# Kernel tuning notes

Measured on AMD Instinct MI355X. Metric: run time of the kernel, lower is better.

Reference implementation:

```python
import jax, jax.numpy as jnp
import numpy as np

NUM_USERS = 100000
NUM_ITEMS = 50000
EMB_DIM = 128
N_EDGES = 1600000
BATCH = 16384
L_USER = (0, 1, 2)


def setup_inputs() -> dict:
    key = jax.random.key(0)
    k1, k2, k3, k4, k5, k6 = jax.random.split(key, 6)
    users = jax.random.randint(k1, (BATCH,), 0, NUM_USERS)
    items = jax.random.randint(k2, (BATCH,), 0, NUM_ITEMS)
    edge_src = jax.random.randint(k3, (N_EDGES,), 0, NUM_USERS)
    edge_dst = jax.random.randint(k4, (N_EDGES,), 0, NUM_USERS)
    # nn.Parameter init: normal(mean=0, std=0.01)
    user_emb = jax.random.normal(k5, (NUM_USERS, EMB_DIM), dtype=jnp.float32) * 0.01
    item_emb = jax.random.normal(k6, (NUM_ITEMS, EMB_DIM), dtype=jnp.float32) * 0.01
    return {"users": users, "items": items, "edge_src": edge_src,
            "edge_dst": edge_dst, "user_emb": user_emb, "item_emb": item_emb}


def social_conv(edge_src, edge_dst, h):
    # DGL copy_u -> mean aggregation over social (user-user) edges
    msgs = h[edge_src]  # [E, D] gather
    agg = jax.ops.segment_sum(msgs, edge_dst, num_segments=NUM_USERS)  # [N, D]
    deg = jax.ops.segment_sum(jnp.ones_like(edge_dst, dtype=h.dtype), edge_dst,
                              num_segments=NUM_USERS)  # [N]
    return agg / jnp.maximum(deg, 1.0)[:, None]


def reference(users, items, edge_src, edge_dst, user_emb, item_emb):
    g1 = social_conv(edge_src, edge_dst, user_emb)
    g2 = social_conv(edge_src, edge_dst, g1)
    final_user = jnp.zeros_like(user_emb)
    if 0 in L_USER:
        final_user = final_user + user_emb
    if 1 in L_USER:
        final_user = final_user + g1
    if 2 in L_USER:
        final_user = final_user + g2
    latest_user = final_user[users]   # [B, D]
    latest_item = item_emb[items]     # [B, D]
    predict = jax.nn.sigmoid(jnp.sum(latest_user * latest_item, axis=1))  # [B]
    return predict, latest_user, latest_item
```

## Files before the change

### kernel.cpp

```cpp
#include <hip/hip_runtime.h>
#include <math.h>

#define NUM_USERS 100000
#define NUM_ITEMS 50000
#define EMB_D 128
#define N_EDGES 1600000
#define BATCH 16384

#define NBINS 782
#define CHUNK 8192
#define NCHUNKS 196
#define CELL 32
#define CAP 64
#define BINSZ (NCHUNKS * CELL)
#define SENT 0xFFFFFFFFu

#define CVT_BLOCKS 782
#define BMAP_BLOCKS 16
#define N_F4 3200000

#define FP8_SCALE 512.0f
#define FP8_INV   (1.0f / 512.0f)

typedef unsigned int u32;
typedef float f32x2 __attribute__((ext_vector_type(2)));

__device__ __forceinline__ long long g18row(int u) {
    return (long long)(u >> 7) * BINSZ + (long long)(u & 127) * 32;
}

__global__ __launch_bounds__(1024) void prep_kernel(const float* __restrict__ in,
                            u32* __restrict__ outp, const int* __restrict__ users,
                            u32* __restrict__ bitmap,
                            const int* __restrict__ edge_src, const int* __restrict__ edge_dst,
                            u32* __restrict__ coarse) {
    int blk = blockIdx.x;
    int tid = threadIdx.x;
    if (blk >= NCHUNKS) {
        int cb = blk - NCHUNKS;
        if (cb < CVT_BLOCKS) {
            long long bbase = (long long)cb * 4096;
            float4 a[4];
            #pragma unroll
            for (int g = 0; g < 4; g++) {
                long long i = bbase + g * 1024 + tid;
                if (i < N_F4) a[g] = ((const float4*)in)[i];
            }
            #pragma unroll
            for (int g = 0; g < 4; g++) {
                long long i = bbase + g * 1024 + tid;
                if (i < N_F4) {
                    int r = __builtin_amdgcn_cvt_pk_fp8_f32(a[g].x * FP8_SCALE,
                                                            a[g].y * FP8_SCALE, 0, false);
                    r = __builtin_amdgcn_cvt_pk_fp8_f32(a[g].z * FP8_SCALE,
                                                        a[g].w * FP8_SCALE, r, true);
                    outp[i] = (u32)r;
                }
            }
        } else {
            int i = (cb - CVT_BLOCKS) * 1024 + tid;
            if (i < BATCH) {
                int u = users[i];
                atomicOr(&bitmap[u >> 5], 1u << (u & 31));
            }
        }
        return;
    }
    extern __shared__ u32 sm[];
    u32* cells = sm;
    int* cnt2  = (int*)(sm + NBINS * CELL);
    for (int i = tid; i < NBINS * CELL; i += 1024) cells[i] = SENT;
    for (int i = tid; i < NBINS; i += 1024) cnt2[i] = 0;
    __syncthreads();
    long long c0 = (long long)blk * CHUNK;
    int n = (int)min((long long)CHUNK, (long long)N_EDGES - c0);
    int n4 = n >> 2;
    const int4* d4p = (const int4*)(edge_dst + c0);
    const int4* s4p = (const int4*)(edge_src + c0);
    for (int i = tid; i < n4; i += 1024) {
        int4 d = d4p[i];
        int4 s = s4p[i];
        int dd[4] = {d.x, d.y, d.z, d.w};
        int ss[4] = {s.x, s.y, s.z, s.w};
        #pragma unroll
        for (int k = 0; k < 4; k++) {
            int b = dd[k] >> 7;
            int idx = atomicAdd(&cnt2[b], 1);
            if (idx < CELL)
                cells[b * CELL + idx] = ((u32)ss[k] << 7) | (u32)(dd[k] & 127);
        }
    }
    __syncthreads();
    const int I4 = NBINS * (CELL / 4);
    for (int i4 = tid; i4 < I4; i4 += 1024) {
        int bin = i4 >> 3;
        int off = i4 & 7;
        *(uint4*)(coarse + (long long)bin * BINSZ + blk * CELL + off * 4) =
            ((const uint4*)cells)[i4];
    }
}

__global__ void binagg_kernel(u32* __restrict__ coarse, const u32* __restrict__ tab32,
                              const u32* __restrict__ bitmap,
                              int* __restrict__ srt, int* __restrict__ counts) {
    __shared__ int cur[128];
    __shared__ int stage[128 * 65];
    int b = blockIdx.x;
    int tid = threadIdx.x;
    if (tid < 128) cur[tid] = 0;
    __syncthreads();
    const uint4* col = (const uint4*)(coarse + (long long)b * BINSZ);
    for (int i4 = tid; i4 < BINSZ / 4; i4 += 512) {
        uint4 q4 = col[i4];
        u32 pv[4] = {q4.x, q4.y, q4.z, q4.w};
        #pragma unroll
        for (int k = 0; k < 4; k++) {
            u32 p = pv[k];
            if (p != SENT) {
                int dl = (int)(p & 127u);
                int pos = atomicAdd(&cur[dl], 1);
                if (pos < CAP) stage[dl * 65 + pos] = (int)(p >> 7);
            }
        }
    }
    __syncthreads();
    int binBase = b << 7;
    int wv = tid >> 6;
    int lane = tid & 63;
    int dlane = lane & 31;
    int hi = lane >> 5;
    for (int dl = wv; dl < 128; dl += 8) {
        int user = binBase + dl;
        if (user >= NUM_USERS) continue;
        int cnt = cur[dl];
        int cl = min(cnt, CAP);
        int sbase = dl * 65;
        float4 acc = make_float4(0.f, 0.f, 0.f, 0.f);
        int j = 0;
        for (; j + 16 <= cl; j += 16) {
            int rr[8];
            #pragma unroll
            for (int k = 0; k < 8; k++) {
                int s0 = stage[sbase + j + 2 * k];
                int s1 = stage[sbase + j + 2 * k + 1];
                rr[k] = hi ? s1 : s0;
            }
            u32 pp[8];
            #pragma unroll
            for (int k = 0; k < 8; k++) pp[k] = tab32[(long long)rr[k] * 32 + dlane];
            #pragma unroll
            for (int k = 0; k < 8; k++) {
                f32x2 d0 = __builtin_amdgcn_cvt_pk_f32_fp8((int)pp[k], false);
                f32x2 d1 = __builtin_amdgcn_cvt_pk_f32_fp8((int)pp[k], true);
                acc.x += d0.x; acc.y += d0.y; acc.z += d1.x; acc.w += d1.y;
            }
        }
        if (j < cl) {
            int rr[8]; float ww[8];
            #pragma unroll
            for (int k = 0; k < 8; k++) {
                int i0 = min(j + 2 * k, cl - 1);
                int i1 = min(j + 2 * k + 1, cl - 1);
                int s0 = stage[sbase + i0];
                int s1 = stage[sbase + i1];
                rr[k] = hi ? s1 : s0;
                ww[k] = ((j + 2 * k + hi) < cl) ? 1.0f : 0.0f;
            }
            u32 pp[8];
            #pragma unroll
            for (int k = 0; k < 8; k++) pp[k] = tab32[(long long)rr[k] * 32 + dlane];
            #pragma unroll
            for (int k = 0; k < 8; k++) {
                f32x2 d0 = __builtin_amdgcn_cvt_pk_f32_fp8((int)pp[k], false);
                f32x2 d1 = __builtin_amdgcn_cvt_pk_f32_fp8((int)pp[k], true);
                acc.x += d0.x * ww[k]; acc.y += d0.y * ww[k];
                acc.z += d1.x * ww[k]; acc.w += d1.y * ww[k];
            }
        }
        acc.x += __shfl_xor(acc.x, 32, 64);
        acc.y += __shfl_xor(acc.y, 32, 64);
        acc.z += __shfl_xor(acc.z, 32, 64);
        acc.w += __shfl_xor(acc.w, 32, 64);
        float inv = 1.0f / fmaxf((float)cnt, 1.0f);
        int enc = __builtin_amdgcn_cvt_pk_fp8_f32(acc.x * inv, acc.y * inv, 0, false);
        enc = __builtin_amdgcn_cvt_pk_fp8_f32(acc.z * inv, acc.w * inv, enc, true);
        if (lane < 32) coarse[g18row(user) + dlane] = (u32)enc;
        if ((bitmap[user >> 5] >> (user & 31)) & 1u)
            srt[(long long)user * CAP + lane] = stage[sbase + lane];
        if (lane == 0) counts[user] = cnt;
    }
}

__global__ void final_kernel(const int* __restrict__ users, const int* __restrict__ items,
                             const float* __restrict__ user_emb, const float* __restrict__ item_emb,
                             const u32* __restrict__ g18, const int* __restrict__ counts,
                             const int* __restrict__ srt,
                             float* __restrict__ out_predict, float* __restrict__ out_lu,
                             float* __restrict__ out_li) {
    int b = (blockIdx.x * blockDim.x + threadIdx.x) >> 6;
    int lane = threadIdx.x & 63;
    if (b >= BATCH) return;
    b = __builtin_amdgcn_readfirstlane(b);
    int u = users[b];
    int it = items[b];
    int cnt = counts[u];
    int cl = min(cnt, CAP);
    long long start = (long long)u * CAP;
    int dlane = lane & 31;
    int hi = lane >> 5;
    float4 acc = make_float4(0.f, 0.f, 0.f, 0.f);
    int j = 0;
    for (; j + 16 <= cl; j += 16) {
        int rr[8];
        #pragma unroll
        for (int k = 0; k < 8; k++) {
            int s0 = srt[start + j + 2 * k];
            int s1 = srt[start + j + 2 * k + 1];
            rr[k] = hi ? s1 : s0;
        }
        u32 pp[8];
        #pragma unroll
        for (int k = 0; k < 8; k++) pp[k] = g18[g18row(rr[k]) + dlane];
        #pragma unroll
        for (int k = 0; k < 8; k++) {
            f32x2 d0 = __builtin_amdgcn_cvt_pk_f32_fp8((int)pp[k], false);
            f32x2 d1 = __builtin_amdgcn_cvt_pk_f32_fp8((int)pp[k], true);
            acc.x += d0.x; acc.y += d0.y; acc.z += d1.x; acc.w += d1.y;
        }
    }
    if (j < cl) {
        int rr[8]; float ww[8];
        #pragma unroll
        for (int k = 0; k < 8; k++) {
            int i0 = min(j + 2 * k, cl - 1);
            int i1 = min(j + 2 * k + 1, cl - 1);
            int s0 = srt[start + i0];
            int s1 = srt[start + i1];
            rr[k] = hi ? s1 : s0;
            ww[k] = ((j + 2 * k + hi) < cl) ? 1.0f : 0.0f;
        }
        u32 pp[8];
        #pragma unroll
        for (int k = 0; k < 8; k++) pp[k] = g18[g18row(rr[k]) + dlane];
        #pragma unroll
        for (int k = 0; k < 8; k++) {
            f32x2 d0 = __builtin_amdgcn_cvt_pk_f32_fp8((int)pp[k], false);
            f32x2 d1 = __builtin_amdgcn_cvt_pk_f32_fp8((int)pp[k], true);
            acc.x += d0.x * ww[k]; acc.y += d0.y * ww[k];
            acc.z += d1.x * ww[k]; acc.w += d1.y * ww[k];
        }
    }
    acc.x += __shfl_xor(acc.x, 32, 64);
    acc.y += __shfl_xor(acc.y, 32, 64);
    acc.z += __shfl_xor(acc.z, 32, 64);
    acc.w += __shfl_xor(acc.w, 32, 64);
    float inv = (1.0f / fmaxf((float)cnt, 1.0f)) * FP8_INV;
    float4 ue = *(const float4*)(user_emb + (long long)u * EMB_D + dlane * 4);
    u32 a1p = g18[g18row(u) + dlane];
    f32x2 a0 = __builtin_amdgcn_cvt_pk_f32_fp8((int)a1p, false);
    f32x2 a1 = __builtin_amdgcn_cvt_pk_f32_fp8((int)a1p, true);
    float4 ie = *(const float4*)(item_emb + (long long)it * EMB_D + dlane * 4);
    float4 lu;
    lu.x = ue.x + a0.x * FP8_INV + acc.x * inv;
    lu.y = ue.y + a0.y * FP8_INV + acc.y * inv;
    lu.z = ue.z + a1.x * FP8_INV + acc.z * inv;
    lu.w = ue.w + a1.y * FP8_INV + acc.w * inv;
    if (lane < 32) {
        *(float4*)(out_lu + (long long)b * EMB_D + dlane * 4) = lu;
        *(float4*)(out_li + (long long)b * EMB_D + dlane * 4) = ie;
    }
    float dot = lu.x * ie.x + lu.y * ie.y + lu.z * ie.z + lu.w * ie.w;
    #pragma unroll
    for (int off = 16; off > 0; off >>= 1) dot += __shfl_down(dot, off, 64);
    if (lane == 0) out_predict[b] = 1.0f / (1.0f + expf(-dot));
}

extern "C" void kernel_launch(void* const* d_in, const int* in_sizes, int n_in,
                              void* d_out, int out_size, void* d_ws, size_t ws_size,
                              hipStream_t stream) {
    const int* users     = (const int*)d_in[0];
    const int* items     = (const int*)d_in[1];
    const int* edge_src  = (const int*)d_in[2];
    const int* edge_dst  = (const int*)d_in[3];
    const float* user_emb = (const float*)d_in[4];
    const float* item_emb = (const float*)d_in[5];

    const long long COARSE_U32 = (long long)NBINS * BINSZ;
    const int SMEM_PART = (NBINS * CELL + NBINS) * 4;

    int* ws_i = (int*)d_ws;
    int* counts = ws_i;
    int* srt    = counts + 100352;
    u32* ue8    = (u32*)(srt + (long long)NUM_USERS * CAP);
    u32* coarse = ue8 + 3200000;
    u32* bitmap = coarse + COARSE_U32;

    float* out_predict = (float*)d_out;
    float* out_lu = out_predict + BATCH;
    float* out_li = out_lu + (long long)BATCH * EMB_D;

    static int lds_set = 0;
    if (!lds_set) {
        hipFuncSetAttribute((const void*)prep_kernel,
                            hipFuncAttributeMaxDynamicSharedMemorySize, SMEM_PART);
        lds_set = 1;
    }

    hipMemsetAsync(bitmap, 0, 3200 * sizeof(u32), stream);

    prep_kernel<<<NCHUNKS + CVT_BLOCKS + BMAP_BLOCKS, 1024, SMEM_PART, stream>>>(
        user_emb, ue8, users, bitmap, edge_src, edge_dst, coarse);

    binagg_kernel<<<NBINS, 512, 0, stream>>>(coarse, ue8, bitmap, srt, counts);

    final_kernel<<<(BATCH + 3) / 4, 256, 0, stream>>>(
        users, items, user_emb, item_emb, coarse, counts, srt,
        out_predict, out_lu, out_li);
}
```

Before: 204.3 us.

## Split bin aggregation into half-bins and compact g1 and neighbor-list storage

The bin aggregation kernel now runs two blocks per destination bin, each handling 64 users, which doubles the grid and halves the shared staging. The cost is that each block reads the whole coarse column and discards half of it. g1 is written to a separate dense fp8 table instead of being folded back into the coarse buffer, so addressing becomes a simple row index. Per-user neighbor lists are stored only for batch users, compacted through a slot map set with atomicMin. This adds a memset and an extra indirection in the final kernel.

```diff
diff --git a/kernel.cpp b/kernel.cpp
--- a/kernel.cpp
+++ b/kernel.cpp
@@ -8,6 +8,7 @@
 #define BATCH 16384
 
 #define NBINS 782
+#define NHALF 1564
 #define CHUNK 8192
 #define NCHUNKS 196
 #define CELL 32
@@ -25,13 +26,9 @@
 typedef unsigned int u32;
 typedef float f32x2 __attribute__((ext_vector_type(2)));
 
-__device__ __forceinline__ long long g18row(int u) {
-    return (long long)(u >> 7) * BINSZ + (long long)(u & 127) * 32;
-}
-
 __global__ __launch_bounds__(1024) void prep_kernel(const float* __restrict__ in,
                             u32* __restrict__ outp, const int* __restrict__ users,
-                            u32* __restrict__ bitmap,
+                            u32* __restrict__ bitmap, int* __restrict__ slot,
                             const int* __restrict__ edge_src, const int* __restrict__ edge_dst,
                             u32* __restrict__ coarse) {
     int blk = blockIdx.x;
@@ -62,6 +59,7 @@
             if (i < BATCH) {
                 int u = users[i];
                 atomicOr(&bitmap[u >> 5], 1u << (u & 31));
+                atomicMin(&slot[u], i);
             }
         }
         return;
@@ -100,16 +98,21 @@
     }
 }
 
-__global__ void binagg_kernel(u32* __restrict__ coarse, const u32* __restrict__ tab32,
-                              const u32* __restrict__ bitmap,
-                              int* __restrict__ srt, int* __restrict__ counts) {
-    __shared__ int cur[128];
-    __shared__ int stage[128 * 65];
+__global__ void binagg_kernel(const u32* __restrict__ coarse, const u32* __restrict__ tab32,
+                              const u32* __restrict__ bitmap, const int* __restrict__ slot,
+                              u32* __restrict__ g18, int* __restrict__ srt,
+                              int* __restrict__ counts) {
+    __shared__ int cur[64];
+    __shared__ int stage[64 * 65];
     int b = blockIdx.x;
+    int bin = b >> 1;
+    int h = b & 1;
+    int binBase = (bin << 7) + (h << 6);
+    if (binBase >= NUM_USERS) return;
     int tid = threadIdx.x;
-    if (tid < 128) cur[tid] = 0;
+    if (tid < 64) cur[tid] = 0;
     __syncthreads();
-    const uint4* col = (const uint4*)(coarse + (long long)b * BINSZ);
+    const uint4* col = (const uint4*)(coarse + (long long)bin * BINSZ);
     for (int i4 = tid; i4 < BINSZ / 4; i4 += 512) {
         uint4 q4 = col[i4];
         u32 pv[4] = {q4.x, q4.y, q4.z, q4.w};
@@ -118,18 +121,20 @@
             u32 p = pv[k];
             if (p != SENT) {
                 int dl = (int)(p & 127u);
-                int pos = atomicAdd(&cur[dl], 1);
-                if (pos < CAP) stage[dl * 65 + pos] = (int)(p >> 7);
+                if ((dl >> 6) == h) {
+                    int d = dl & 63;
+                    int pos = atomicAdd(&cur[d], 1);
+                    if (pos < CAP) stage[d * 65 + pos] = (int)(p >> 7);
+                }
             }
         }
     }
     __syncthreads();
-    int binBase = b << 7;
     int wv = tid >> 6;
     int lane = tid & 63;
     int dlane = lane & 31;
     int hi = lane >> 5;
-    for (int dl = wv; dl < 128; dl += 8) {
+    for (int dl = wv; dl < 64; dl += 8) {
         int user = binBase + dl;
         if (user >= NUM_USERS) continue;
         int cnt = cur[dl];
@@ -184,9 +189,11 @@
         float inv = 1.0f / fmaxf((float)cnt, 1.0f);
         int enc = __builtin_amdgcn_cvt_pk_fp8_f32(acc.x * inv, acc.y * inv, 0, false);
         enc = __builtin_amdgcn_cvt_pk_fp8_f32(acc.z * inv, acc.w * inv, enc, true);
-        if (lane < 32) coarse[g18row(user) + dlane] = (u32)enc;
-        if ((bitmap[user >> 5] >> (user & 31)) & 1u)
-            srt[(long long)user * CAP + lane] = stage[sbase + lane];
+        if (lane < 32) g18[(long long)user * 32 + dlane] = (u32)enc;
+        if ((bitmap[user >> 5] >> (user & 31)) & 1u) {
+            int s = slot[user];
+            srt[(long long)s * CAP + lane] = stage[sbase + lane];
+        }
         if (lane == 0) counts[user] = cnt;
     }
 }
@@ -194,7 +201,7 @@
 __global__ void final_kernel(const int* __restrict__ users, const int* __restrict__ items,
                              const float* __restrict__ user_emb, const float* __restrict__ item_emb,
                              const u32* __restrict__ g18, const int* __restrict__ counts,
-                             const int* __restrict__ srt,
+                             const int* __restrict__ slot, const int* __restrict__ srt,
                              float* __restrict__ out_predict, float* __restrict__ out_lu,
                              float* __restrict__ out_li) {
     int b = (blockIdx.x * blockDim.x + threadIdx.x) >> 6;
@@ -205,7 +212,7 @@
     int it = items[b];
     int cnt = counts[u];
     int cl = min(cnt, CAP);
-    long long start = (long long)u * CAP;
+    long long start = (long long)slot[u] * CAP;
     int dlane = lane & 31;
     int hi = lane >> 5;
     float4 acc = make_float4(0.f, 0.f, 0.f, 0.f);
@@ -220,7 +227,7 @@
         }
         u32 pp[8];
         #pragma unroll
-        for (int k = 0; k < 8; k++) pp[k] = g18[g18row(rr[k]) + dlane];
+        for (int k = 0; k < 8; k++) pp[k] = g18[(long long)rr[k] * 32 + dlane];
         #pragma unroll
         for (int k = 0; k < 8; k++) {
             f32x2 d0 = __builtin_amdgcn_cvt_pk_f32_fp8((int)pp[k], false);
@@ -241,7 +248,7 @@
         }
         u32 pp[8];
         #pragma unroll
-        for (int k = 0; k < 8; k++) pp[k] = g18[g18row(rr[k]) + dlane];
+        for (int k = 0; k < 8; k++) pp[k] = g18[(long long)rr[k] * 32 + dlane];
         #pragma unroll
         for (int k = 0; k < 8; k++) {
             f32x2 d0 = __builtin_amdgcn_cvt_pk_f32_fp8((int)pp[k], false);
@@ -256,7 +263,7 @@
     acc.w += __shfl_xor(acc.w, 32, 64);
     float inv = (1.0f / fmaxf((float)cnt, 1.0f)) * FP8_INV;
     float4 ue = *(const float4*)(user_emb + (long long)u * EMB_D + dlane * 4);
-    u32 a1p = g18[g18row(u) + dlane];
+    u32 a1p = g18[(long long)u * 32 + dlane];
     f32x2 a0 = __builtin_amdgcn_cvt_pk_f32_fp8((int)a1p, false);
     f32x2 a1 = __builtin_amdgcn_cvt_pk_f32_fp8((int)a1p, true);
     float4 ie = *(const float4*)(item_emb + (long long)it * EMB_D + dlane * 4);
@@ -290,10 +297,12 @@
 
     int* ws_i = (int*)d_ws;
     int* counts = ws_i;
-    int* srt    = counts + 100352;
-    u32* ue8    = (u32*)(srt + (long long)NUM_USERS * CAP);
+    int* slot   = counts + 100352;
+    int* srt    = slot + 100352;
+    u32* ue8    = (u32*)(srt + (long long)BATCH * CAP);
     u32* coarse = ue8 + 3200000;
-    u32* bitmap = coarse + COARSE_U32;
+    u32* g18    = coarse + COARSE_U32;
+    u32* bitmap = g18 + 3200000;
 
     float* out_predict = (float*)d_out;
     float* out_lu = out_predict + BATCH;
@@ -307,13 +316,14 @@
     }
 
     hipMemsetAsync(bitmap, 0, 3200 * sizeof(u32), stream);
+    hipMemsetAsync(slot, 0x7f, 100352 * sizeof(int), stream);
 
     prep_kernel<<<NCHUNKS + CVT_BLOCKS + BMAP_BLOCKS, 1024, SMEM_PART, stream>>>(
-        user_emb, ue8, users, bitmap, edge_src, edge_dst, coarse);
-
-    binagg_kernel<<<NBINS, 512, 0, stream>>>(coarse, ue8, bitmap, srt, counts);
+        user_emb, ue8, users, bitmap, slot, edge_src, edge_dst, coarse);
+
+    binagg_kernel<<<NHALF, 512, 0, stream>>>(coarse, ue8, bitmap, slot, g18, srt, counts);
 
     final_kernel<<<(BATCH + 3) / 4, 256, 0, stream>>>(
-        users, items, user_emb, item_emb, coarse, counts, srt,
+        users, items, user_emb, item_emb, g18, counts, slot, srt,
         out_predict, out_lu, out_li);
 }
```

Result: no change. 201.7 us (-1.3%).
